# Kernel optimization log

Measured on AMD Instinct MI355X. Metric: run time of the kernel, lower is better.

Reference implementation:

```python
import jax, jax.numpy as jnp
import numpy as np

D_MODEL = 1024
NUM_HEADS = 16
DILATION = 2
SEG = 2048


def setup_inputs() -> dict:
    key = jax.random.key(0)
    k1, k2, k3, k4, k5 = jax.random.split(key, 5)
    B, S, D = 2, 8192, D_MODEL
    scale = 1.0 / np.sqrt(D)
    x = jax.random.normal(k1, (B, S, D), dtype=jnp.float32)
    wqkv = jax.random.normal(k2, (D, 3 * D), dtype=jnp.float32) * scale
    bqkv = jnp.zeros((3 * D,), dtype=jnp.float32)
    wo = jax.random.normal(k3, (D, D), dtype=jnp.float32) * scale
    bo = jnp.zeros((D,), dtype=jnp.float32)
    return {"x": x, "wqkv": wqkv, "bqkv": bqkv, "wo": wo, "bo": bo}


def reference(x, wqkv, bqkv, wo, bo):
    B, S, D = x.shape
    H = NUM_HEADS
    hd = D // H
    # segment reshape + dilated strided slice: [B, N, L, D]
    xs = x.reshape(B, -1, SEG, D)[:, :, ::DILATION, :]
    Bn, N, L, _ = xs.shape
    # fused QKV projection
    qkv = xs @ wqkv + bqkv                       # [B, N, L, 3D]
    q, k, v = jnp.split(qkv, 3, axis=-1)
    q = q.reshape(B, N, L, H, hd)
    k = k.reshape(B, N, L, H, hd)
    v = v.reshape(B, N, L, H, hd)
    scale = 1.0 / jnp.sqrt(jnp.asarray(hd, dtype=x.dtype))
    scores = jnp.einsum("bnqhd,bnkhd->bnhqk", q, k) * scale
    attn = jax.nn.softmax(scores, axis=-1)
    out = jnp.einsum("bnhqk,bnkhd->bnqhd", attn, v).reshape(B, N, L, D)
    out = out @ wo + bo                          # out projection
    return out.reshape(B, N * L, D)
```

## Files before the change

### kernel.cpp

```cpp
#include <hip/hip_runtime.h>
#include <hip/hip_bf16.h>
#include <stdint.h>

typedef __attribute__((ext_vector_type(8))) short short8;
typedef __attribute__((ext_vector_type(4))) float float4v;
typedef __attribute__((ext_vector_type(4))) unsigned int uint4v;
typedef unsigned short u16;

#if __has_builtin(__builtin_amdgcn_exp2f)
#define EXP2F(x) __builtin_amdgcn_exp2f(x)
#else
#define EXP2F(x) __expf(0.69314718056f * (x))
#endif

__device__ __forceinline__ u16 f2b(float f) {
    union { __hip_bfloat16 b; u16 u; } cv;
    cv.b = __float2bfloat16(f);
    return cv.u;
}

#define GLD16(g, l) __builtin_amdgcn_global_load_lds( \
    (const __attribute__((address_space(1))) void*)(g), \
    (__attribute__((address_space(3))) void*)(l), 16, 0, 0)

__global__ __launch_bounds__(256) void prep(const float* __restrict__ x, u16* __restrict__ xb,
                                            const float* __restrict__ wqkv, u16* __restrict__ wqkvT,
                                            const float* __restrict__ wo, u16* __restrict__ woT) {
    const int bx = blockIdx.x;
    const int tid = threadIdx.x;
    if (bx < 8192) {
        int id = bx * 256 + tid;
        int row = id >> 8;
        int c4 = id & 255;
        const float4* src = reinterpret_cast<const float4*>(x + (size_t)(2 * row) * 1024) + c4;
        float4 v = *src;
        ushort4 o;
        o.x = f2b(v.x); o.y = f2b(v.y); o.z = f2b(v.z); o.w = f2b(v.w);
        *(reinterpret_cast<ushort4*>(xb + (size_t)row * 1024) + c4) = o;
        return;
    }
    __shared__ float tile[32][33];
    const float* in;
    u16* out;
    int n0, k0, N;
    if (bx < 8192 + 3072) {
        int bb = bx - 8192;
        in = wqkv; out = wqkvT; N = 3072;
        n0 = (bb % 96) * 32; k0 = (bb / 96) * 32;
    } else {
        int bb = bx - 11264;
        in = wo; out = woT; N = 1024;
        n0 = (bb & 31) * 32; k0 = (bb >> 5) * 32;
    }
    int tx = tid & 31, ty = tid >> 5;
#pragma unroll
    for (int i = 0; i < 4; i++)
        tile[ty + i * 8][tx] = in[(size_t)(k0 + ty + i * 8) * N + n0 + tx];
    __syncthreads();
#pragma unroll
    for (int i = 0; i < 4; i++)
        out[(size_t)(n0 + ty + i * 8) * 1024 + k0 + tx] = f2b(tile[tx][ty + i * 8]);
}

template <int MODE>
__global__ __launch_bounds__(256) void gemm_bt(
    const u16* __restrict__ A, const u16* __restrict__ BT,
    const float* __restrict__ bias,
    float* __restrict__ Cf, u16* __restrict__ Cqk, u16* __restrict__ Cvt,
    int M, int N, int K) {
    __shared__ u16 As[128 * 64];
    __shared__ u16 Bs[128 * 64];
    const int tid = threadIdx.x;
    const int w = tid >> 6, l = tid & 63;
    const int q = l >> 4, c = l & 15;
    const int m0 = blockIdx.y * 128, n0 = blockIdx.x * 128;
    const int wm = (w >> 1) * 64, wn = (w & 1) * 64;

    const int srow = w * 8 + (l >> 3);
    const int scol = ((l & 7) ^ (srow & 7)) * 8;
    const u16* gA = A + (size_t)(m0 + srow) * K + scol;
    const u16* gB = BT + (size_t)(n0 + srow) * K + scol;
    char* AsB = (char*)&As[0];
    char* BsB = (char*)&Bs[0];
    const int ldsOff = (w * 8) * 128;

    float4v acc[4][4];
#pragma unroll
    for (int i = 0; i < 4; i++)
#pragma unroll
        for (int j = 0; j < 4; j++) acc[i][j] = {0.f, 0.f, 0.f, 0.f};

    const int cs = c & 7;

    for (int k0 = 0; k0 < K; k0 += 64) {
        __syncthreads();
#pragma unroll
        for (int j = 0; j < 4; j++) {
            GLD16(gA + (size_t)(j * 32) * K + k0, AsB + ldsOff + j * 32 * 128);
            GLD16(gB + (size_t)(j * 32) * K + k0, BsB + ldsOff + j * 32 * 128);
        }
        __syncthreads();
#pragma unroll
        for (int kk = 0; kk < 2; kk++) {
            const int phys = ((kk * 4 + q) ^ cs) * 8;
            short8 af[4], bf[4];
#pragma unroll
            for (int mt = 0; mt < 4; mt++)
                af[mt] = *reinterpret_cast<const short8*>(&As[(wm + mt * 16 + c) * 64 + phys]);
#pragma unroll
            for (int nt = 0; nt < 4; nt++)
                bf[nt] = *reinterpret_cast<const short8*>(&Bs[(wn + nt * 16 + c) * 64 + phys]);
#pragma unroll
            for (int mt = 0; mt < 4; mt++)
#pragma unroll
                for (int nt = 0; nt < 4; nt++)
                    acc[mt][nt] = __builtin_amdgcn_mfma_f32_16x16x32_bf16(af[mt], bf[nt], acc[mt][nt], 0, 0, 0);
        }
    }

    const int q4 = q * 4;
    if (MODE == 0) {
#pragma unroll
        for (int nt = 0; nt < 4; nt++) {
            int col = n0 + wn + nt * 16 + c;
            float bv = bias[col];
#pragma unroll
            for (int mt = 0; mt < 4; mt++) {
                int row = m0 + wm + mt * 16 + q4;
#pragma unroll
                for (int r = 0; r < 4; r++)
                    Cf[(size_t)(row + r) * N + col] = acc[mt][nt][r] + bv;
            }
        }
    } else {
        bool isV = (n0 + wn) >= 2048;
        float qscale = ((n0 + wn) < 1024) ? (0.125f * 1.44269504f) : 1.0f;
#pragma unroll
        for (int nt = 0; nt < 4; nt++) {
            int col = n0 + wn + nt * 16 + c;
            float bv = bias[col];
            if (!isV) {
#pragma unroll
                for (int mt = 0; mt < 4; mt++) {
                    int row = m0 + wm + mt * 16 + q4;
#pragma unroll
                    for (int r = 0; r < 4; r++)
                        Cqk[(size_t)(row + r) * 2048 + col] = f2b((acc[mt][nt][r] + bv) * qscale);
                }
            } else {
                int hd_ = col - 2048;
#pragma unroll
                for (int mt = 0; mt < 4; mt++) {
                    int row = m0 + wm + mt * 16 + q4;
                    int bn = row >> 10, key = row & 1023;
                    ushort4 pk;
                    pk.x = f2b(acc[mt][nt][0] + bv);
                    pk.y = f2b(acc[mt][nt][1] + bv);
                    pk.z = f2b(acc[mt][nt][2] + bv);
                    pk.w = f2b(acc[mt][nt][3] + bv);
                    *reinterpret_cast<ushort4*>(
                        &Cvt[((size_t)(bn << 10) + hd_) * 1024 + key]) = pk;
                }
            }
        }
    }
}

__global__ __launch_bounds__(256) void attn(const u16* __restrict__ qk,
                                            const u16* __restrict__ vt,
                                            u16* __restrict__ ob) {
    __shared__ u16 Ks[64 * 72];
    __shared__ u16 Vs[64 * 72];
    __shared__ u16 Ps[64 * 72];
    const int tid = threadIdx.x;
    const int w = tid >> 6, l = tid & 63, q = l >> 4, c = l & 15;
    const int combo = blockIdx.x, qtile = blockIdx.y;
    const int bn = combo >> 4, h = combo & 15;
    const int t0 = bn << 10;
    const int qoff = h << 6;
    const int koff = 1024 + (h << 6);
    const int vrow0 = combo << 6;
    const int qrow_base = t0 + qtile * 64 + w * 16;

    short8 v1;
    {
        u16 one = (c == 0) ? (u16)0x3F80 : (u16)0;
#pragma unroll
        for (int j = 0; j < 8; j++) v1[j] = (short)one;
    }

    short8 aq[2];
#pragma unroll
    for (int ks = 0; ks < 2; ks++)
        aq[ks] = *reinterpret_cast<const short8*>(
            qk + (size_t)(qrow_base + c) * 2048 + qoff + ks * 32 + q * 8);

    float4v o_acc[4];
    float4v osum = {0.f, 0.f, 0.f, 0.f};
#pragma unroll
    for (int nt = 0; nt < 4; nt++) o_acc[nt] = {0.f, 0.f, 0.f, 0.f};

    const int sr = tid >> 3;
    const int sc = (tid & 7) * 8;

    uint4v kreg[2], vreg[2];
#pragma unroll
    for (int i = 0; i < 2; i++) {
        int r = sr + i * 32;
        kreg[i] = *reinterpret_cast<const uint4v*>(
            qk + (size_t)(t0 + r) * 2048 + koff + sc);
        vreg[i] = *reinterpret_cast<const uint4v*>(
            vt + (size_t)(vrow0 + r) * 1024 + sc);
    }
#pragma unroll
    for (int i = 0; i < 2; i++) {
        int r = sr + i * 32;
        *reinterpret_cast<uint4v*>(&Ks[r * 72 + sc]) = kreg[i];
        *reinterpret_cast<uint4v*>(&Vs[r * 72 + sc]) = vreg[i];
    }
    __syncthreads();

    for (int chunk = 0; chunk < 16; chunk++) {
        if (chunk < 15) {
            const int key0n = (chunk + 1) * 64;
#pragma unroll
            for (int i = 0; i < 2; i++) {
                int r = sr + i * 32;
                kreg[i] = *reinterpret_cast<const uint4v*>(
                    qk + (size_t)(t0 + key0n + r) * 2048 + koff + sc);
                vreg[i] = *reinterpret_cast<const uint4v*>(
                    vt + (size_t)(vrow0 + r) * 1024 + key0n + sc);
            }
        }

        float4v s[4];
#pragma unroll
        for (int nt = 0; nt < 4; nt++) s[nt] = {0.f, 0.f, 0.f, 0.f};
#pragma unroll
        for (int ks = 0; ks < 2; ks++) {
            short8 bk[4];
#pragma unroll
            for (int nt = 0; nt < 4; nt++)
                bk[nt] = *reinterpret_cast<const short8*>(&Ks[(nt * 16 + c) * 72 + ks * 32 + q * 8]);
#pragma unroll
            for (int nt = 0; nt < 4; nt++)
                s[nt] = __builtin_amdgcn_mfma_f32_16x16x32_bf16(aq[ks], bk[nt], s[nt], 0, 0, 0);
        }

#pragma unroll
        for (int r = 0; r < 4; r++)
#pragma unroll
            for (int nt = 0; nt < 4; nt++)
                Ps[(w * 16 + q * 4 + r) * 72 + nt * 16 + c] = f2b(EXP2F(s[nt][r]));

#pragma unroll
        for (int ks = 0; ks < 2; ks++) {
            short8 pf, vf[4];
            pf = *reinterpret_cast<const short8*>(&Ps[(w * 16 + c) * 72 + ks * 32 + q * 8]);
#pragma unroll
            for (int nt = 0; nt < 4; nt++)
                vf[nt] = *reinterpret_cast<const short8*>(&Vs[(nt * 16 + c) * 72 + ks * 32 + q * 8]);
#pragma unroll
            for (int nt = 0; nt < 4; nt++)
                o_acc[nt] = __builtin_amdgcn_mfma_f32_16x16x32_bf16(pf, vf[nt], o_acc[nt], 0, 0, 0);
            osum = __builtin_amdgcn_mfma_f32_16x16x32_bf16(pf, v1, osum, 0, 0, 0);
        }

        if (chunk < 15) {
            __syncthreads();
#pragma unroll
            for (int i = 0; i < 2; i++) {
                int r = sr + i * 32;
                *reinterpret_cast<uint4v*>(&Ks[r * 72 + sc]) = kreg[i];
                *reinterpret_cast<uint4v*>(&Vs[r * 72 + sc]) = vreg[i];
            }
            __syncthreads();
        }
    }

    float inv[4];
#pragma unroll
    for (int r = 0; r < 4; r++) {
        float lv = __shfl(osum[r], tid & 48);
        inv[r] = 1.0f / lv;
    }
#pragma unroll
    for (int nt = 0; nt < 4; nt++)
#pragma unroll
        for (int r = 0; r < 4; r++) {
            int row = qrow_base + q * 4 + r;
            int col = (h << 6) + nt * 16 + c;
            ob[(size_t)row * 1024 + col] = f2b(o_acc[nt][r] * inv[r]);
        }
}

extern "C" void kernel_launch(void* const* d_in, const int* in_sizes, int n_in,
                              void* d_out, int out_size, void* d_ws, size_t ws_size,
                              hipStream_t stream) {
    const float* x    = (const float*)d_in[0];
    const float* wqkv = (const float*)d_in[1];
    const float* bqkv = (const float*)d_in[2];
    const float* wo   = (const float*)d_in[3];
    const float* bo   = (const float*)d_in[4];
    float* out = (float*)d_out;
    char* ws = (char*)d_ws;

    u16* xb    = (u16*)(ws);
    u16* wqkvT = (u16*)(ws + 16777216);
    u16* woT   = (u16*)(ws + 23068672);
    u16* qkb   = (u16*)(ws + 25165824);
    u16* vtb   = (u16*)(ws + 58720256);
    u16* obuf  = (u16*)(ws + 75497472);

    prep<<<12288, 256, 0, stream>>>(x, xb, wqkv, wqkvT, wo, woT);
    gemm_bt<1><<<dim3(24, 64), 256, 0, stream>>>(xb, wqkvT, bqkv,
                                                 nullptr, qkb, vtb, 8192, 3072, 1024);
    attn<<<dim3(128, 16), 256, 0, stream>>>(qkb, vtb, obuf);
    gemm_bt<0><<<dim3(8, 64), 256, 0, stream>>>(obuf, woT, bo,
                                                out, nullptr, nullptr, 8192, 1024, 1024);
}
```

Before: 268.9 us.

## Enlarge attention query tile to 128 rows with 2 waves of 64 rows each

The attention kernel now runs 2 waves per block, each handling four 16-row query sub-tiles (64 rows), so every K/V chunk staged in LDS feeds 128 query rows instead of 64. This halves K/V global loads and LDS staging per query and raises the MFMA-to-LDS-read ratio, since each K/V fragment is reused across four m-tiles. The P buffer gets padded row offsets to reduce bank conflicts. In exchange the register footprint grows considerably, the grid is halved, and fewer waves per block leaves less latency hiding per block.

```diff
diff --git a/kernel.cpp b/kernel.cpp
--- a/kernel.cpp
+++ b/kernel.cpp
@@ -22,6 +22,8 @@
 #define GLD16(g, l) __builtin_amdgcn_global_load_lds( \
     (const __attribute__((address_space(1))) void*)(g), \
     (__attribute__((address_space(3))) void*)(l), 16, 0, 0)
+
+#define PS_OFF(row) ((row) * 72 + ((row) >> 2) * 8)
 
 __global__ __launch_bounds__(256) void prep(const float* __restrict__ x, u16* __restrict__ xb,
                                             const float* __restrict__ wqkv, u16* __restrict__ wqkvT,
@@ -166,12 +168,12 @@
     }
 }
 
-__global__ __launch_bounds__(256) void attn(const u16* __restrict__ qk,
+__global__ __launch_bounds__(128) void attn(const u16* __restrict__ qk,
                                             const u16* __restrict__ vt,
                                             u16* __restrict__ ob) {
     __shared__ u16 Ks[64 * 72];
     __shared__ u16 Vs[64 * 72];
-    __shared__ u16 Ps[64 * 72];
+    __shared__ u16 Ps[128 * 72 + 32 * 8];
     const int tid = threadIdx.x;
     const int w = tid >> 6, l = tid & 63, q = l >> 4, c = l & 15;
     const int combo = blockIdx.x, qtile = blockIdx.y;
@@ -180,7 +182,8 @@
     const int qoff = h << 6;
     const int koff = 1024 + (h << 6);
     const int vrow0 = combo << 6;
-    const int qrow_base = t0 + qtile * 64 + w * 16;
+    const int wrow = w * 64;
+    const int qrow_base = t0 + qtile * 128 + wrow;
 
     short8 v1;
     {
@@ -189,32 +192,38 @@
         for (int j = 0; j < 8; j++) v1[j] = (short)one;
     }
 
-    short8 aq[2];
-#pragma unroll
-    for (int ks = 0; ks < 2; ks++)
-        aq[ks] = *reinterpret_cast<const short8*>(
-            qk + (size_t)(qrow_base + c) * 2048 + qoff + ks * 32 + q * 8);
-
-    float4v o_acc[4];
-    float4v osum = {0.f, 0.f, 0.f, 0.f};
-#pragma unroll
-    for (int nt = 0; nt < 4; nt++) o_acc[nt] = {0.f, 0.f, 0.f, 0.f};
+    short8 aq[4][2];
+#pragma unroll
+    for (int mt = 0; mt < 4; mt++)
+#pragma unroll
+        for (int ks = 0; ks < 2; ks++)
+            aq[mt][ks] = *reinterpret_cast<const short8*>(
+                qk + (size_t)(qrow_base + mt * 16 + c) * 2048 + qoff + ks * 32 + q * 8);
+
+    float4v o_acc[4][4];
+    float4v osum[4];
+#pragma unroll
+    for (int mt = 0; mt < 4; mt++) {
+#pragma unroll
+        for (int nt = 0; nt < 4; nt++) o_acc[mt][nt] = {0.f, 0.f, 0.f, 0.f};
+        osum[mt] = {0.f, 0.f, 0.f, 0.f};
+    }
 
     const int sr = tid >> 3;
     const int sc = (tid & 7) * 8;
 
-    uint4v kreg[2], vreg[2];
-#pragma unroll
-    for (int i = 0; i < 2; i++) {
-        int r = sr + i * 32;
+    uint4v kreg[4], vreg[4];
+#pragma unroll
+    for (int i = 0; i < 4; i++) {
+        int r = sr + i * 16;
         kreg[i] = *reinterpret_cast<const uint4v*>(
             qk + (size_t)(t0 + r) * 2048 + koff + sc);
         vreg[i] = *reinterpret_cast<const uint4v*>(
             vt + (size_t)(vrow0 + r) * 1024 + sc);
     }
 #pragma unroll
-    for (int i = 0; i < 2; i++) {
-        int r = sr + i * 32;
+    for (int i = 0; i < 4; i++) {
+        int r = sr + i * 16;
         *reinterpret_cast<uint4v*>(&Ks[r * 72 + sc]) = kreg[i];
         *reinterpret_cast<uint4v*>(&Vs[r * 72 + sc]) = vreg[i];
     }
@@ -224,8 +233,8 @@
         if (chunk < 15) {
             const int key0n = (chunk + 1) * 64;
 #pragma unroll
-            for (int i = 0; i < 2; i++) {
-                int r = sr + i * 32;
+            for (int i = 0; i < 4; i++) {
+                int r = sr + i * 16;
                 kreg[i] = *reinterpret_cast<const uint4v*>(
                     qk + (size_t)(t0 + key0n + r) * 2048 + koff + sc);
                 vreg[i] = *reinterpret_cast<const uint4v*>(
@@ -233,9 +242,11 @@
             }
         }
 
-        float4v s[4];
-#pragma unroll
-        for (int nt = 0; nt < 4; nt++) s[nt] = {0.f, 0.f, 0.f, 0.f};
+        float4v s[4][4];
+#pragma unroll
+        for (int mt = 0; mt < 4; mt++)
+#pragma unroll
+            for (int nt = 0; nt < 4; nt++) s[mt][nt] = {0.f, 0.f, 0.f, 0.f};
 #pragma unroll
         for (int ks = 0; ks < 2; ks++) {
             short8 bk[4];
@@ -243,34 +254,45 @@
             for (int nt = 0; nt < 4; nt++)
                 bk[nt] = *reinterpret_cast<const short8*>(&Ks[(nt * 16 + c) * 72 + ks * 32 + q * 8]);
 #pragma unroll
-            for (int nt = 0; nt < 4; nt++)
-                s[nt] = __builtin_amdgcn_mfma_f32_16x16x32_bf16(aq[ks], bk[nt], s[nt], 0, 0, 0);
-        }
-
-#pragma unroll
-        for (int r = 0; r < 4; r++)
-#pragma unroll
-            for (int nt = 0; nt < 4; nt++)
-                Ps[(w * 16 + q * 4 + r) * 72 + nt * 16 + c] = f2b(EXP2F(s[nt][r]));
+            for (int mt = 0; mt < 4; mt++)
+#pragma unroll
+                for (int nt = 0; nt < 4; nt++)
+                    s[mt][nt] = __builtin_amdgcn_mfma_f32_16x16x32_bf16(aq[mt][ks], bk[nt], s[mt][nt], 0, 0, 0);
+        }
+
+#pragma unroll
+        for (int mt = 0; mt < 4; mt++)
+#pragma unroll
+            for (int r = 0; r < 4; r++)
+#pragma unroll
+                for (int nt = 0; nt < 4; nt++)
+                    Ps[PS_OFF(wrow + mt * 16 + q * 4 + r) + nt * 16 + c] =
+                        f2b(EXP2F(s[mt][nt][r]));
 
 #pragma unroll
         for (int ks = 0; ks < 2; ks++) {
-            short8 pf, vf[4];
-            pf = *reinterpret_cast<const short8*>(&Ps[(w * 16 + c) * 72 + ks * 32 + q * 8]);
+            short8 pf[4], vf[4];
+#pragma unroll
+            for (int mt = 0; mt < 4; mt++)
+                pf[mt] = *reinterpret_cast<const short8*>(
+                    &Ps[PS_OFF(wrow + mt * 16 + c) + ks * 32 + q * 8]);
 #pragma unroll
             for (int nt = 0; nt < 4; nt++)
                 vf[nt] = *reinterpret_cast<const short8*>(&Vs[(nt * 16 + c) * 72 + ks * 32 + q * 8]);
 #pragma unroll
-            for (int nt = 0; nt < 4; nt++)
-                o_acc[nt] = __builtin_amdgcn_mfma_f32_16x16x32_bf16(pf, vf[nt], o_acc[nt], 0, 0, 0);
-            osum = __builtin_amdgcn_mfma_f32_16x16x32_bf16(pf, v1, osum, 0, 0, 0);
+            for (int mt = 0; mt < 4; mt++) {
+#pragma unroll
+                for (int nt = 0; nt < 4; nt++)
+                    o_acc[mt][nt] = __builtin_amdgcn_mfma_f32_16x16x32_bf16(pf[mt], vf[nt], o_acc[mt][nt], 0, 0, 0);
+                osum[mt] = __builtin_amdgcn_mfma_f32_16x16x32_bf16(pf[mt], v1, osum[mt], 0, 0, 0);
+            }
         }
 
         if (chunk < 15) {
             __syncthreads();
 #pragma unroll
-            for (int i = 0; i < 2; i++) {
-                int r = sr + i * 32;
+            for (int i = 0; i < 4; i++) {
+                int r = sr + i * 16;
                 *reinterpret_cast<uint4v*>(&Ks[r * 72 + sc]) = kreg[i];
                 *reinterpret_cast<uint4v*>(&Vs[r * 72 + sc]) = vreg[i];
             }
@@ -278,20 +300,23 @@
         }
     }
 
-    float inv[4];
-#pragma unroll
-    for (int r = 0; r < 4; r++) {
-        float lv = __shfl(osum[r], tid & 48);
-        inv[r] = 1.0f / lv;
-    }
-#pragma unroll
-    for (int nt = 0; nt < 4; nt++)
+#pragma unroll
+    for (int mt = 0; mt < 4; mt++) {
+        float inv[4];
 #pragma unroll
         for (int r = 0; r < 4; r++) {
-            int row = qrow_base + q * 4 + r;
-            int col = (h << 6) + nt * 16 + c;
-            ob[(size_t)row * 1024 + col] = f2b(o_acc[nt][r] * inv[r]);
-        }
+            float lv = __shfl(osum[mt][r], tid & 48);
+            inv[r] = 1.0f / lv;
+        }
+#pragma unroll
+        for (int nt = 0; nt < 4; nt++)
+#pragma unroll
+            for (int r = 0; r < 4; r++) {
+                int row = qrow_base + mt * 16 + q * 4 + r;
+                int col = (h << 6) + nt * 16 + c;
+                ob[(size_t)row * 1024 + col] = f2b(o_acc[mt][nt][r] * inv[r]);
+            }
+    }
 }
 
 extern "C" void kernel_launch(void* const* d_in, const int* in_sizes, int n_in,
@@ -315,7 +340,7 @@
     prep<<<12288, 256, 0, stream>>>(x, xb, wqkv, wqkvT, wo, woT);
     gemm_bt<1><<<dim3(24, 64), 256, 0, stream>>>(xb, wqkvT, bqkv,
                                                  nullptr, qkb, vtb, 8192, 3072, 1024);
-    attn<<<dim3(128, 16), 256, 0, stream>>>(qkb, vtb, obuf);
+    attn<<<dim3(128, 8), 128, 0, stream>>>(qkb, vtb, obuf);
     gemm_bt<0><<<dim3(8, 64), 256, 0, stream>>>(obuf, woT, bo,
                                                 out, nullptr, nullptr, 8192, 1024, 1024);
 }
```

Measured after the change: 278.2 us. +3.5%, slower.
